# Kernel optimization log

Hardware: AMD Instinct MI355X
Metric: run time of the kernel (lower is better)

The kernel has to match this reference:

```python
import jax, jax.numpy as jnp
import numpy as np

X_MIN, X_MAX = -2.0, 2.0


def _pchip_slopes_uniform(y, h):
    # y: [..., K], uniform knot spacing h. Fritsch-Carlson / PCHIP slopes.
    delta = (y[..., 1:] - y[..., :-1]) / h            # [..., K-1]
    dp, dn = delta[..., :-1], delta[..., 1:]          # [..., K-2]
    same_sign = dp * dn > 0
    d_mid = jnp.where(same_sign, 2.0 * dp * dn / (dp + dn + 1e-12), 0.0)

    def _fix_endpoint(d_end, delta0, delta1):
        d_end = jnp.where(d_end * delta0 <= 0, 0.0, d_end)
        d_end = jnp.where((delta0 * delta1 < 0) & (jnp.abs(d_end) > 3.0 * jnp.abs(delta0)),
                          3.0 * delta0, d_end)
        return d_end

    d0 = _fix_endpoint((3.0 * delta[..., 0] - delta[..., 1]) / 2.0, delta[..., 0], delta[..., 1])
    dN = _fix_endpoint((3.0 * delta[..., -1] - delta[..., -2]) / 2.0, delta[..., -1], delta[..., -2])
    return jnp.concatenate([d0[..., None], d_mid, dN[..., None]], axis=-1)


def setup_inputs() -> dict:
    key = jax.random.key(0)
    k1, k2 = jax.random.split(key)
    B, O, D, K = 8192, 64, 64, 64
    x = jax.random.normal(k1, (B, D), dtype=jnp.float32)
    coeffs = 0.01 * jax.random.normal(k2, (O, D, K), dtype=jnp.float32)
    bias = jnp.zeros((O,), dtype=jnp.float32)
    return {"x": x, "coeffs": coeffs, "bias": bias}


def reference(x, coeffs, bias):
    # x: [B, D]; coeffs: [O, D, K]; bias: [O] -> out: [B, O]
    O, D, K = coeffs.shape
    h = (X_MAX - X_MIN) / (K - 1)
    slopes = _pchip_slopes_uniform(coeffs, h)          # [O, D, K]

    t = (x - X_MIN) / h                                # [B, D]
    idx = jnp.clip(jnp.floor(t).astype(jnp.int32), 0, K - 2)
    u = (t - idx)[None]                                # [1, B, D]

    darange = jnp.arange(D)[None, :]                   # broadcasts with idx [B, D]
    y0 = coeffs[:, darange, idx]                       # [O, B, D]
    y1 = coeffs[:, darange, idx + 1]
    d0 = slopes[:, darange, idx]
    d1 = slopes[:, darange, idx + 1]

    u2 = u * u
    u3 = u2 * u
    h00 = 2.0 * u3 - 3.0 * u2 + 1.0
    h10 = u3 - 2.0 * u2 + u
    h01 = -2.0 * u3 + 3.0 * u2
    h11 = u3 - u2
    interp = h00 * y0 + h10 * (h * d0) + h01 * y1 + h11 * (h * d1)  # [O, B, D]

    # linear extrapolation outside [X_MIN, X_MAX]
    left = coeffs[:, :, 0][:, None, :] + slopes[:, :, 0][:, None, :] * (x - X_MIN)[None]
    right = coeffs[:, :, -1][:, None, :] + slopes[:, :, -1][:, None, :] * (x - X_MAX)[None]
    interp = jnp.where((x < X_MIN)[None], left, interp)
    interp = jnp.where((x > X_MAX)[None], right, interp)

    out = interp.sum(axis=-1).T + bias[None, :]        # [B, O]
    return out
```

## Files before the change

kernel.cpp:

```cpp
#include <hip/hip_runtime.h>
#include <stdint.h>


__device__ __forceinline__ uint32_t bf16r(float f) {
    uint32_t u = __float_as_uint(f);
    return (u + 0x7fffu + ((u >> 16) & 1u)) >> 16;
}

__global__ void build_table(const float* __restrict__ coeffs, uint2* __restrict__ T) {
    const float hf = 4.0f / 63.0f;
    const float inv_hf = 63.0f / 4.0f;
    int d  = blockIdx.x >> 2;
    int ob = (blockIdx.x & 3) << 4;
    __shared__ float Y[16][65];
    int t = threadIdx.x;
    {
        int ol = t >> 4;
        int k4 = (t & 15) << 2;
        const float* src = coeffs + (size_t)(ob + ol) * 4096 + d * 64 + k4;
        float4 v = *(const float4*)src;
        Y[ol][k4 + 0] = v.x; Y[ol][k4 + 1] = v.y;
        Y[ol][k4 + 2] = v.z; Y[ol][k4 + 3] = v.w;
    }
    __syncthreads();
    for (int c = t; c < 1024; c += 256) {
        int ol = c & 15;
        int i  = c >> 4;
        const float* Yr = Y[ol];
        auto delt = [&](int k) -> float { return (Yr[k + 1] - Yr[k]) * inv_hf; };
        auto endslope = [&](float a, float b) -> float {
            float de = (3.0f * a - b) * 0.5f;
            de = (de * a <= 0.0f) ? 0.0f : de;
            de = ((a * b < 0.0f) && (fabsf(de) > 3.0f * fabsf(a))) ? 3.0f * a : de;
            return de;
        };
        auto slope = [&](int k) -> float {
            if (k == 0)  return endslope(delt(0), delt(1));
            if (k == 63) return endslope(delt(62), delt(61));
            float dp = delt(k - 1), dn = delt(k);
            return (dp * dn > 0.0f) ? (2.0f * dp * dn) / (dp + dn + 1e-12f) : 0.0f;
        };
        uint2 pk;
        if (i < 63) {
            float y0 = Yr[i], y1 = Yr[i + 1];
            float di = slope(i), dj = slope(i + 1);
            float c0 = y0;
            float c1 = hf * di;
            float c2 = 3.0f * (y1 - y0) - hf * (2.0f * di + dj);
            float c3 = 2.0f * (y0 - y1) + hf * (di + dj);
            pk.x = (bf16r(c1) << 16) | bf16r(c0);
            pk.y = (bf16r(c3) << 16) | bf16r(c2);
        } else {
            float yN = Yr[63];
            float dN = slope(63);
            pk.x = (bf16r(hf * dN) << 16) | bf16r(yN);
            pk.y = 0u;
        }
        T[(size_t)d * 4096 + i * 64 + (ob + ol)] = pk;
    }
}

__global__ void __launch_bounds__(1024) kan_main(const float* __restrict__ x,
                                                 const float* __restrict__ bias,
                                                 const char* __restrict__ Tb,
                                                 float* __restrict__ out) {
    __shared__ uint4 WrecL[1024];
    const float hf = 4.0f / 63.0f;
    int t  = threadIdx.x;
    int bx = blockIdx.x;

    {
        float xv = x[(size_t)bx * 1024 + t];
        float tt = (xv + 2.0f) / hf;
        int i = (int)floorf(tt);
        i = i < 0 ? 0 : (i > 62 ? 62 : i);
        float u = tt - (float)i;
        float w1, w2, w3; uint32_t off;
        if (xv < -2.0f)      { w1 = tt;          w2 = 0.0f;  w3 = 0.0f;  off = 0u; }
        else if (xv > 2.0f)  { w1 = tt - 63.0f;  w2 = 0.0f;  w3 = 0.0f;  off = 63u << 9; }
        else                 { w1 = u;           w2 = u * u; w3 = w2 * u; off = (uint32_t)i << 9; }
        WrecL[t] = make_uint4(__float_as_uint(w1), __float_as_uint(w2),
                              __float_as_uint(w3), off);
    }
    __syncthreads();

    int w    = __builtin_amdgcn_readfirstlane(t >> 6);
    int lane = t & 63;
    int rowq = w & 3;
    int dq   = w >> 2;
    int laneoff = lane << 3;
    float acc0 = 0.f, acc1 = 0.f, acc2 = 0.f, acc3 = 0.f;
    const char* slice = Tb + (size_t)dq * 16 * 32768;
    int wbase = rowq * 4 * 64 + (dq << 4);
    for (int dd = 0; dd < 16; ++dd) {
        uint4 q0 = WrecL[wbase + 0 * 64 + dd];
        uint4 q1 = WrecL[wbase + 1 * 64 + dd];
        uint4 q2 = WrecL[wbase + 2 * 64 + dd];
        uint4 q3 = WrecL[wbase + 3 * 64 + dd];
        uint2 p0 = *(const uint2*)(slice + q0.w + laneoff);
        uint2 p1 = *(const uint2*)(slice + q1.w + laneoff);
        uint2 p2 = *(const uint2*)(slice + q2.w + laneoff);
        uint2 p3 = *(const uint2*)(slice + q3.w + laneoff);

        acc0 += __uint_as_float(p0.x << 16);
        acc0 = fmaf(__uint_as_float(q0.x), __uint_as_float(p0.x & 0xffff0000u), acc0);
        acc0 = fmaf(__uint_as_float(q0.y), __uint_as_float(p0.y << 16),         acc0);
        acc0 = fmaf(__uint_as_float(q0.z), __uint_as_float(p0.y & 0xffff0000u), acc0);

        acc1 += __uint_as_float(p1.x << 16);
        acc1 = fmaf(__uint_as_float(q1.x), __uint_as_float(p1.x & 0xffff0000u), acc1);
        acc1 = fmaf(__uint_as_float(q1.y), __uint_as_float(p1.y << 16),         acc1);
        acc1 = fmaf(__uint_as_float(q1.z), __uint_as_float(p1.y & 0xffff0000u), acc1);

        acc2 += __uint_as_float(p2.x << 16);
        acc2 = fmaf(__uint_as_float(q2.x), __uint_as_float(p2.x & 0xffff0000u), acc2);
        acc2 = fmaf(__uint_as_float(q2.y), __uint_as_float(p2.y << 16),         acc2);
        acc2 = fmaf(__uint_as_float(q2.z), __uint_as_float(p2.y & 0xffff0000u), acc2);

        acc3 += __uint_as_float(p3.x << 16);
        acc3 = fmaf(__uint_as_float(q3.x), __uint_as_float(p3.x & 0xffff0000u), acc3);
        acc3 = fmaf(__uint_as_float(q3.y), __uint_as_float(p3.y << 16),         acc3);
        acc3 = fmaf(__uint_as_float(q3.z), __uint_as_float(p3.y & 0xffff0000u), acc3);

        slice += 32768;
    }
    __syncthreads();

    float* Obuf = (float*)WrecL;
    int obase = dq * 1024 + rowq * 4 * 64 + lane;
    Obuf[obase + 0 * 64] = acc0;
    Obuf[obase + 1 * 64] = acc1;
    Obuf[obase + 2 * 64] = acc2;
    Obuf[obase + 3 * 64] = acc3;
    __syncthreads();
    float s = Obuf[t] + Obuf[1024 + t] + Obuf[2048 + t] + Obuf[3072 + t];
    out[(size_t)bx * 1024 + t] = s + bias[t & 63];
}

extern "C" void kernel_launch(void* const* d_in, const int* in_sizes, int n_in,
                              void* d_out, int out_size, void* d_ws, size_t ws_size,
                              hipStream_t stream) {
    const float* x      = (const float*)d_in[0];
    const float* coeffs = (const float*)d_in[1];
    const float* bias   = (const float*)d_in[2];
    float* out = (float*)d_out;

    uint2* T = (uint2*)d_ws;
    build_table<<<dim3(256), dim3(256), 0, stream>>>(coeffs, T);
    kan_main<<<dim3(512), dim3(1024), 0, stream>>>(x, bias, (const char*)d_ws, out);
}
```

Before: 80.05 us.

## Store spline table in fp16 and accumulate with packed dot2 instructions

The table coefficients switch from bf16 to fp16, and the Hermite polynomial is evaluated with two packed fp16 dot-product (fdot2) instructions per knot instead of unpacking bf16 and issuing four FMAs. The main kernel is restructured so each wave handles one batch row across all 64 input dims, with 256-thread blocks and no cross-wave LDS reduction. The aim is to cut ALU work per lookup and remove the reduction and barriers. In exchange, the u powers are rounded to fp16, which costs accuracy, and the per-wave work is more serial.

```diff
diff --git a/kernel.cpp b/kernel.cpp
--- a/kernel.cpp
+++ b/kernel.cpp
@@ -1,10 +1,28 @@
 #include <hip/hip_runtime.h>
+#include <hip/hip_fp16.h>
 #include <stdint.h>
 
 
-__device__ __forceinline__ uint32_t bf16r(float f) {
-    uint32_t u = __float_as_uint(f);
-    return (u + 0x7fffu + ((u >> 16) & 1u)) >> 16;
+typedef _Float16 half2v __attribute__((ext_vector_type(2)));
+
+#if defined(__has_builtin)
+#if __has_builtin(__builtin_amdgcn_fdot2)
+#define HAS_FDOT2 1
+#endif
+#endif
+
+__device__ __forceinline__ uint32_t h16(float f) {
+    return (uint32_t)__half_as_ushort(__float2half(f));
+}
+
+__device__ __forceinline__ float dot2acc(uint32_t a_bits, uint32_t b_bits, float acc) {
+    half2v a = __builtin_bit_cast(half2v, a_bits);
+    half2v b = __builtin_bit_cast(half2v, b_bits);
+#ifdef HAS_FDOT2
+    return __builtin_amdgcn_fdot2(a, b, acc, false);
+#else
+    return acc + (float)a.x * (float)b.x + (float)a.y * (float)b.y;
+#endif
 }
 
 __global__ void build_table(const float* __restrict__ coeffs, uint2* __restrict__ T) {
@@ -48,93 +66,59 @@
             float c1 = hf * di;
             float c2 = 3.0f * (y1 - y0) - hf * (2.0f * di + dj);
             float c3 = 2.0f * (y0 - y1) + hf * (di + dj);
-            pk.x = (bf16r(c1) << 16) | bf16r(c0);
-            pk.y = (bf16r(c3) << 16) | bf16r(c2);
+            pk.x = (h16(c1) << 16) | h16(c0);
+            pk.y = (h16(c3) << 16) | h16(c2);
         } else {
             float yN = Yr[63];
             float dN = slope(63);
-            pk.x = (bf16r(hf * dN) << 16) | bf16r(yN);
+            pk.x = (h16(hf * dN) << 16) | h16(yN);
             pk.y = 0u;
         }
         T[(size_t)d * 4096 + i * 64 + (ob + ol)] = pk;
     }
 }
 
-__global__ void __launch_bounds__(1024) kan_main(const float* __restrict__ x,
-                                                 const float* __restrict__ bias,
-                                                 const char* __restrict__ Tb,
-                                                 float* __restrict__ out) {
-    __shared__ uint4 WrecL[1024];
-    const float hf = 4.0f / 63.0f;
-    int t  = threadIdx.x;
-    int bx = blockIdx.x;
+__global__ void __launch_bounds__(256) kan_main(const float* __restrict__ x,
+                                                const float* __restrict__ bias,
+                                                const char* __restrict__ Tb,
+                                                float* __restrict__ out) {
+    __shared__ uint4 WL[256];
+    int t    = threadIdx.x;
+    int lane = t & 63;
+    int wv   = t >> 6;
+    int b    = blockIdx.x * 4 + wv;
 
     {
-        float xv = x[(size_t)bx * 1024 + t];
-        float tt = (xv + 2.0f) / hf;
+        float xv = x[b * 64 + lane];
+        float tt = (xv + 2.0f) * 15.75f;
         int i = (int)floorf(tt);
         i = i < 0 ? 0 : (i > 62 ? 62 : i);
         float u = tt - (float)i;
         float w1, w2, w3; uint32_t off;
-        if (xv < -2.0f)      { w1 = tt;          w2 = 0.0f;  w3 = 0.0f;  off = 0u; }
-        else if (xv > 2.0f)  { w1 = tt - 63.0f;  w2 = 0.0f;  w3 = 0.0f;  off = 63u << 9; }
-        else                 { w1 = u;           w2 = u * u; w3 = w2 * u; off = (uint32_t)i << 9; }
-        WrecL[t] = make_uint4(__float_as_uint(w1), __float_as_uint(w2),
-                              __float_as_uint(w3), off);
+        if (xv < -2.0f)      { w1 = tt;          w2 = 0.f;    w3 = 0.f;    off = 0u; }
+        else if (xv > 2.0f)  { w1 = tt - 63.0f;  w2 = 0.f;    w3 = 0.f;    off = 63u << 9; }
+        else                 { w1 = u;           w2 = u * u;  w3 = w2 * u; off = (uint32_t)i << 9; }
+        half2v wa; wa.x = (_Float16)1.0f; wa.y = (_Float16)w1;
+        half2v wb; wb.x = (_Float16)w2;   wb.y = (_Float16)w3;
+        uint32_t full_off = ((uint32_t)lane << 15) | off;
+        WL[t] = make_uint4(__builtin_bit_cast(uint32_t, wa),
+                           __builtin_bit_cast(uint32_t, wb), full_off, 0u);
     }
     __syncthreads();
 
-    int w    = __builtin_amdgcn_readfirstlane(t >> 6);
-    int lane = t & 63;
-    int rowq = w & 3;
-    int dq   = w >> 2;
+    float acc0 = bias[lane];
+    float acc1 = 0.0f;
     int laneoff = lane << 3;
-    float acc0 = 0.f, acc1 = 0.f, acc2 = 0.f, acc3 = 0.f;
-    const char* slice = Tb + (size_t)dq * 16 * 32768;
-    int wbase = rowq * 4 * 64 + (dq << 4);
-    for (int dd = 0; dd < 16; ++dd) {
-        uint4 q0 = WrecL[wbase + 0 * 64 + dd];
-        uint4 q1 = WrecL[wbase + 1 * 64 + dd];
-        uint4 q2 = WrecL[wbase + 2 * 64 + dd];
-        uint4 q3 = WrecL[wbase + 3 * 64 + dd];
-        uint2 p0 = *(const uint2*)(slice + q0.w + laneoff);
-        uint2 p1 = *(const uint2*)(slice + q1.w + laneoff);
-        uint2 p2 = *(const uint2*)(slice + q2.w + laneoff);
-        uint2 p3 = *(const uint2*)(slice + q3.w + laneoff);
-
-        acc0 += __uint_as_float(p0.x << 16);
-        acc0 = fmaf(__uint_as_float(q0.x), __uint_as_float(p0.x & 0xffff0000u), acc0);
-        acc0 = fmaf(__uint_as_float(q0.y), __uint_as_float(p0.y << 16),         acc0);
-        acc0 = fmaf(__uint_as_float(q0.z), __uint_as_float(p0.y & 0xffff0000u), acc0);
-
-        acc1 += __uint_as_float(p1.x << 16);
-        acc1 = fmaf(__uint_as_float(q1.x), __uint_as_float(p1.x & 0xffff0000u), acc1);
-        acc1 = fmaf(__uint_as_float(q1.y), __uint_as_float(p1.y << 16),         acc1);
-        acc1 = fmaf(__uint_as_float(q1.z), __uint_as_float(p1.y & 0xffff0000u), acc1);
-
-        acc2 += __uint_as_float(p2.x << 16);
-        acc2 = fmaf(__uint_as_float(q2.x), __uint_as_float(p2.x & 0xffff0000u), acc2);
-        acc2 = fmaf(__uint_as_float(q2.y), __uint_as_float(p2.y << 16),         acc2);
-        acc2 = fmaf(__uint_as_float(q2.z), __uint_as_float(p2.y & 0xffff0000u), acc2);
-
-        acc3 += __uint_as_float(p3.x << 16);
-        acc3 = fmaf(__uint_as_float(q3.x), __uint_as_float(p3.x & 0xffff0000u), acc3);
-        acc3 = fmaf(__uint_as_float(q3.y), __uint_as_float(p3.y << 16),         acc3);
-        acc3 = fmaf(__uint_as_float(q3.z), __uint_as_float(p3.y & 0xffff0000u), acc3);
-
-        slice += 32768;
+    const uint4* wl = &WL[wv << 6];
+    #pragma unroll 8
+    for (int d = 0; d < 64; ++d) {
+        uint4 q = wl[d];
+        uint32_t off = __builtin_amdgcn_readfirstlane(q.z);
+        uint2 c = *(const uint2*)(Tb + off + laneoff);
+        acc0 = dot2acc(q.x, c.x, acc0);
+        acc1 = dot2acc(q.y, c.y, acc1);
     }
-    __syncthreads();
-
-    float* Obuf = (float*)WrecL;
-    int obase = dq * 1024 + rowq * 4 * 64 + lane;
-    Obuf[obase + 0 * 64] = acc0;
-    Obuf[obase + 1 * 64] = acc1;
-    Obuf[obase + 2 * 64] = acc2;
-    Obuf[obase + 3 * 64] = acc3;
-    __syncthreads();
-    float s = Obuf[t] + Obuf[1024 + t] + Obuf[2048 + t] + Obuf[3072 + t];
-    out[(size_t)bx * 1024 + t] = s + bias[t & 63];
+    out[b * 64 + lane] = acc0 + acc1;
 }
 
 extern "C" void kernel_launch(void* const* d_in, const int* in_sizes, int n_in,
@@ -147,5 +131,5 @@
 
     uint2* T = (uint2*)d_ws;
     build_table<<<dim3(256), dim3(256), 0, stream>>>(coeffs, T);
-    kan_main<<<dim3(512), dim3(1024), 0, stream>>>(x, bias, (const char*)d_ws, out);
+    kan_main<<<dim3(2048), dim3(256), 0, stream>>>(x, bias, (const char*)d_ws, out);
 }
```

Measured after the change: 78.57 us. About the same (-1.8%).
